# Optimization experiments

Measured on AMD Instinct MI355X. Metric: run time of the kernel, lower is better.

Reference implementation:

```python
import jax, jax.numpy as jnp
import numpy as np

B, C, H, W = 2, 256, 128, 128
G, S = 2, 4  # group_num, stride


def setup_inputs() -> dict:
    key = jax.random.key(0)
    ks = jax.random.split(key, 6)
    x = jax.random.normal(ks[0], (B, C, H, W), jnp.float32)
    qkv_w = jax.random.normal(ks[1], (C + C // 2, C), jnp.float32) * 0.02
    qkv_b = jax.random.normal(ks[2], (C + C // 2,), jnp.float32) * 0.02
    out_w = jax.random.normal(ks[3], (C, C), jnp.float32) * 0.02
    out_b = jax.random.normal(ks[4], (C,), jnp.float32) * 0.02
    gamma = jax.random.normal(ks[5], (1,), jnp.float32) * 0.1
    return {"x": x, "qkv_w": qkv_w, "qkv_b": qkv_b, "out_w": out_w,
            "out_b": out_b, "gamma": gamma, "mode": 0}


def reference(x, qkv_w, qkv_b, out_w, out_b, gamma, mode):
    b, c, h, w = x.shape
    g, s = G, S
    b1, c1, c2 = b * g, c // 4 // g, c // g
    h1, w1 = h // s, w // s
    n1, n = h1 * w1, h * w
    # 1x1 QKV conv
    qkv = jnp.einsum('oc,bchw->bohw', qkv_w, x) + qkv_b[None, :, None, None]
    Q = qkv[:, :c // 4]
    K = qkv[:, c // 4:c // 2]
    V = qkv[:, c // 2:]
    # avg_pool2d with kernel=stride=s (non-overlapping) via reshape-mean
    pool = lambda t: t.reshape(b, c // 4, h1, s, w1, s).mean(axis=(3, 5))
    q = pool(Q).reshape(b1, c1, n1)
    k = pool(K).reshape(b1, c1, n1)
    Qf = Q.reshape(b1, c1, n)
    Kf = K.reshape(b1, c1, n)
    Vf = V.reshape(b1, c2, n)
    # attention maps; softmax over dim=1 (the row / key index)
    A_c = jax.nn.softmax(jnp.einsum('bki,bkj->bij', k, Qf), axis=1)   # [b1,n1,n]
    A_m = jax.nn.softmax(jnp.einsum('bki,bkj->bij', k, q), axis=1)    # [b1,n1,n1]
    A_s = jax.nn.softmax(jnp.einsum('bki,bkj->bij', Kf, q), axis=1)   # [b1,n,n1]
    e = jnp.eye(n1, dtype=x.dtype)
    # E: each pooled-token identity row expanded over its s x s spatial block
    E = jnp.broadcast_to(e.reshape(n1, h1, 1, w1, 1),
                         (n1, h1, s, w1, s)).reshape(n1, n)
    A_c = jnp.linalg.inv(A_m + e) @ (A_c + E)                          # [b1,n1,n]
    O = (Vf @ A_s) @ A_c                                               # [b1,c2,n]
    out = O.reshape(b, c, h, w)
    out = jnp.einsum('oc,bchw->bohw', out_w, out) + out_b[None, :, None, None]
    if mode == 0:
        out = gamma[0] * out + x
    return out
```

## Files before the change

### kernel.cpp

```cpp
#include <hip/hip_runtime.h>
#include <cstdint>
#include <cstddef>

#define HWN 16384
#define NP1 1024
#define RL2E 1.44269504f

typedef __attribute__((ext_vector_type(8))) short bf16x8;
typedef __attribute__((ext_vector_type(8))) unsigned short ushort8v;
typedef __attribute__((ext_vector_type(4))) unsigned short ushort4v;
typedef __attribute__((ext_vector_type(2))) unsigned int uint2v;
typedef __attribute__((ext_vector_type(4))) unsigned int uint4v;
typedef __attribute__((ext_vector_type(4))) float f32x4;

__device__ __forceinline__ unsigned short f2bu(float f) {
  unsigned int u = __builtin_bit_cast(unsigned int, f);
  u = (u + 0x7FFFu + ((u >> 16) & 1u)) >> 16;
  return (unsigned short)u;
}
__device__ __forceinline__ float b2f(unsigned short s) {
  unsigned int u = ((unsigned int)s) << 16;
  return __builtin_bit_cast(float, u);
}
__device__ __forceinline__ unsigned cvtpk(float lo, float hi) {
  unsigned r;
  asm("v_cvt_pk_bf16_f32 %0, %1, %2" : "=v"(r) : "v"(lo), "v"(hi));
  return r;
}
__device__ __forceinline__ bf16x8 scale_l2e(ushort8v t) {
  ushort8v o;
#pragma unroll
  for (int q = 0; q < 8; ++q) o[q] = f2bu(RL2E * b2f(t[q]));
  return __builtin_bit_cast(bf16x8, o);
}
#define MFMA16(A,B,C) __builtin_amdgcn_mfma_f32_16x16x32_bf16((A),(B),(C),0,0,0)
#define PIDX(r,c) ((((r) << 6) + (c)) ^ (((r) & 7) << 3))

__global__ __launch_bounds__(256) void k_cast(
    const float* __restrict__ x, const float* __restrict__ qkv_w,
    const float* __restrict__ out_w, unsigned short* __restrict__ xbT,
    unsigned short* __restrict__ wqb, unsigned short* __restrict__ wob) {
  int bid = blockIdx.x, t = threadIdx.x;
  if (bid < 2048) {
    __shared__ float Lt[64][65];
    int b = bid >> 10, rest = bid & 1023, ct = rest >> 8, pt = rest & 255;
    const float* xp = x + ((size_t)b * 256 + ct * 64) * HWN + pt * 64;
    for (int it = 0; it < 16; ++it) {
      int idx = it * 256 + t; int cc = idx >> 6, pp = idx & 63;
      Lt[cc][pp] = xp[(size_t)cc * HWN + pp];
    }
    __syncthreads();
    int prow = t >> 2, c0 = (t & 3) * 16;
    unsigned short* dst = xbT + ((size_t)b * HWN + pt * 64 + prow) * 256 + ct * 64 + c0;
    uint4v o1, o2;
#pragma unroll
    for (int q = 0; q < 4; ++q) o1[q] = cvtpk(Lt[c0 + 2*q][prow], Lt[c0 + 2*q + 1][prow]);
#pragma unroll
    for (int q = 0; q < 4; ++q) o2[q] = cvtpk(Lt[c0 + 8 + 2*q][prow], Lt[c0 + 9 + 2*q][prow]);
    *(uint4v*)dst = o1;
    *(uint4v*)(dst + 8) = o2;
  } else {
    int base = (bid - 2048) * 1024 + t * 4;
    if (base < 98304) {
      float4 v = *(const float4*)(qkv_w + base);
      uint2v o; o[0] = cvtpk(v.x, v.y); o[1] = cvtpk(v.z, v.w);
      *(uint2v*)(wqb + base) = o;
    } else {
      int b2 = base - 98304;
      float4 v = *(const float4*)(out_w + b2);
      uint2v o; o[0] = cvtpk(v.x, v.y); o[1] = cvtpk(v.z, v.w);
      *(uint2v*)(wob + b2) = o;
    }
  }
}

__global__ __launch_bounds__(256) void k_qkv(
    const unsigned short* __restrict__ wqb, const unsigned short* __restrict__ xbT,
    const float* __restrict__ qkv_b, unsigned short* __restrict__ qkvb,
    unsigned short* __restrict__ kT) {
  int pt = blockIdx.x, b = blockIdx.y;
  int tid = threadIdx.x, w = tid >> 6, lane = tid & 63;
  int lg = lane >> 4, ln = lane & 15;
  f32x4 acc[6][4] = {};
#pragma unroll
  for (int ks = 0; ks < 8; ++ks) {
    int c0 = ks * 32;
    bf16x8 bx[4];
#pragma unroll
    for (int nt = 0; nt < 4; ++nt)
      bx[nt] = *(const bf16x8*)(xbT + ((size_t)b * HWN + pt * 64 + nt * 16 + ln) * 256 + c0 + lg * 8);
#pragma unroll
    for (int ot = 0; ot < 6; ++ot) {
      bf16x8 aw = *(const bf16x8*)(wqb + (size_t)(ot * 64 + w * 16 + ln) * 256 + c0 + lg * 8);
#pragma unroll
      for (int nt = 0; nt < 4; ++nt)
        acc[ot][nt] = MFMA16(aw, bx[nt], acc[ot][nt]);
    }
  }
#pragma unroll
  for (int ot = 0; ot < 6; ++ot) {
    int ob = ot * 64 + w * 16 + lg * 4;
    float b0 = qkv_b[ob], b1 = qkv_b[ob + 1], b2 = qkv_b[ob + 2], b3 = qkv_b[ob + 3];
#pragma unroll
    for (int nt = 0; nt < 4; ++nt) {
      int p = pt * 64 + nt * 16 + ln;
      unsigned u01 = cvtpk(acc[ot][nt][0] + b0, acc[ot][nt][1] + b1);
      unsigned u23 = cvtpk(acc[ot][nt][2] + b2, acc[ot][nt][3] + b3);
      size_t qb = ((size_t)b * 384 + ob) * HWN + p;
      qkvb[qb]           = (unsigned short)u01;
      qkvb[qb + HWN]     = (unsigned short)(u01 >> 16);
      qkvb[qb + 2 * HWN] = (unsigned short)u23;
      qkvb[qb + 3 * HWN] = (unsigned short)(u23 >> 16);
      if (ot == 1) {
        int bgi = b * 2 + (w >> 1);
        int d0 = (w & 1) * 16 + lg * 4;
        uint2v kv; kv[0] = u01; kv[1] = u23;
        *(uint2v*)(kT + ((size_t)bgi * HWN + p) * 32 + d0) = kv;
      }
    }
  }
}

__global__ __launch_bounds__(256) void k_pool(
    const unsigned short* __restrict__ qkvb, unsigned short* __restrict__ qpb,
    unsigned short* __restrict__ kpt) {
  int idx = blockIdx.x * 256 + threadIdx.x;
  int i1 = idx & 1023, cc = (idx >> 10) & 31, bg = idx >> 15;
  int b = bg >> 1, g = bg & 1;
  int h1 = i1 >> 5, w1 = i1 & 31;
  const unsigned short* bq = qkvb + (size_t)(b * 384 + g * 32 + cc) * HWN;
  const unsigned short* bk = qkvb + (size_t)(b * 384 + 64 + g * 32 + cc) * HWN;
  float sq = 0.f, sk = 0.f;
#pragma unroll
  for (int sh = 0; sh < 4; ++sh) {
    int off = (h1 * 4 + sh) * 128 + w1 * 4;
    ushort4v vq = *(const ushort4v*)(bq + off);
    ushort4v vk = *(const ushort4v*)(bk + off);
#pragma unroll
    for (int e = 0; e < 4; ++e) { sq += b2f(vq[e]); sk += b2f(vk[e]); }
  }
  qpb[((size_t)bg * 32 + cc) * NP1 + i1] = f2bu(sq * 0.0625f);
  kpt[((size_t)bg * NP1 + i1) * 32 + cc] = f2bu(sk * 0.0625f);
}

__global__ __launch_bounds__(256) void k_fw1s(
    const unsigned short* __restrict__ qkvb, const unsigned short* __restrict__ kT,
    const unsigned short* __restrict__ qpb, const unsigned short* __restrict__ kpt,
    float* __restrict__ pacc, float* __restrict__ pl,
    unsigned short* __restrict__ Eut, float* __restrict__ lpart) {
  __shared__ unsigned short PtS[2][64 * 64];
  __shared__ float redL[4][64];
  int n = blockIdx.x;
  int tid = threadIdx.x, w = tid >> 6, lane = tid & 63;
  int lg = lane >> 4, ln = lane & 15;

  if (n < 512) {
    int wid = ((n & 7) << 6) + (n >> 3);
    int jt = wid & 15, kc = (wid >> 4) & 7, bg = wid >> 7;
    int b = bg >> 1, g = bg & 1;
    const int Vch = b * 384 + 128 + g * 128;
    bf16x8 bq[4];
#pragma unroll
    for (int nt = 0; nt < 4; ++nt) {
      ushort8v t8;
#pragma unroll
      for (int jr = 0; jr < 8; ++jr)
        t8[jr] = qpb[((size_t)bg * 32 + lg * 8 + jr) * NP1 + jt * 64 + nt * 16 + ln];
      bq[nt] = scale_l2e(t8);
    }
    f32x4 acc[2][4] = {};
    float lsum[4] = {0.f, 0.f, 0.f, 0.f};
    const int i0base = kc * 2048;
    const unsigned short* kTbase = kT + ((size_t)bg * HWN + i0base + w * 16 + ln) * 32 + lg * 8;
    const unsigned short* Vrow0 = qkvb + (size_t)(Vch + w * 32 + ln) * HWN + i0base + lg * 8;
    const unsigned short* Vrow1 = qkvb + (size_t)(Vch + w * 32 + 16 + ln) * HWN + i0base + lg * 8;

    bf16x8 akA, akB;
    bf16x8 avA[4], avB[4];
    akA = *(const bf16x8*)(kTbase);
    {
      f32x4 sn[4];
#pragma unroll
      for (int nt = 0; nt < 4; ++nt) { f32x4 z = {0.f,0.f,0.f,0.f}; sn[nt] = MFMA16(akA, bq[nt], z); }
      akB = *(const bf16x8*)(kTbase + 2048);
      avA[0] = *(const bf16x8*)(Vrow0);
      avA[1] = *(const bf16x8*)(Vrow1);
      avA[2] = *(const bf16x8*)(Vrow0 + 32);
      avA[3] = *(const bf16x8*)(Vrow1 + 32);
#pragma unroll
      for (int nt = 0; nt < 4; ++nt) {
        float e0 = exp2f(sn[nt][0]), e1 = exp2f(sn[nt][1]), e2 = exp2f(sn[nt][2]), e3 = exp2f(sn[nt][3]);
        lsum[nt] += (e0 + e1) + (e2 + e3);
        uint2v pk; pk[0] = cvtpk(e0, e1); pk[1] = cvtpk(e2, e3);
        *(uint2v*)&PtS[0][PIDX(nt * 16 + ln, w * 16 + lg * 4)] = pk;
      }
    }
    for (int pr = 0; pr < 16; ++pr) {
      int c = pr * 2;
      __syncthreads();
      f32x4 sn[4];
#pragma unroll
      for (int nt = 0; nt < 4; ++nt) { f32x4 z = {0.f,0.f,0.f,0.f}; sn[nt] = MFMA16(akB, bq[nt], z); }
      {
        int c2 = (c + 2) & 31, c1 = c + 1;
        akA = *(const bf16x8*)(kTbase + (size_t)c2 * 2048);
        avB[0] = *(const bf16x8*)(Vrow0 + c1 * 64);
        avB[1] = *(const bf16x8*)(Vrow1 + c1 * 64);
        avB[2] = *(const bf16x8*)(Vrow0 + c1 * 64 + 32);
        avB[3] = *(const bf16x8*)(Vrow1 + c1 * 64 + 32);
      }
      __builtin_amdgcn_s_setprio(1);
#pragma unroll
      for (int ist = 0; ist < 2; ++ist) {
        bf16x8 bp[4];
#pragma unroll
        for (int nt = 0; nt < 4; ++nt)
          bp[nt] = *(const bf16x8*)&PtS[0][PIDX(nt * 16 + ln, ist * 32 + lg * 8)];
#pragma unroll
        for (int nt = 0; nt < 4; ++nt) {
          acc[0][nt] = MFMA16(avA[ist * 2 + 0], bp[nt], acc[0][nt]);
          acc[1][nt] = MFMA16(avA[ist * 2 + 1], bp[nt], acc[1][nt]);
        }
      }
      __builtin_amdgcn_s_setprio(0);
#pragma unroll
      for (int nt = 0; nt < 4; ++nt) {
        float e0 = exp2f(sn[nt][0]), e1 = exp2f(sn[nt][1]), e2 = exp2f(sn[nt][2]), e3 = exp2f(sn[nt][3]);
        lsum[nt] += (e0 + e1) + (e2 + e3);
        uint2v pk; pk[0] = cvtpk(e0, e1); pk[1] = cvtpk(e2, e3);
        *(uint2v*)&PtS[1][PIDX(nt * 16 + ln, w * 16 + lg * 4)] = pk;
      }
      __syncthreads();
      if (pr < 15) {
#pragma unroll
        for (int nt = 0; nt < 4; ++nt) { f32x4 z = {0.f,0.f,0.f,0.f}; sn[nt] = MFMA16(akA, bq[nt], z); }
        int c3 = c + 3, c2 = c + 2;
        akB = *(const bf16x8*)(kTbase + (size_t)c3 * 2048);
        avA[0] = *(const bf16x8*)(Vrow0 + c2 * 64);
        avA[1] = *(const bf16x8*)(Vrow1 + c2 * 64);
        avA[2] = *(const bf16x8*)(Vrow0 + c2 * 64 + 32);
        avA[3] = *(const bf16x8*)(Vrow1 + c2 * 64 + 32);
      }
      __builtin_amdgcn_s_setprio(1);
#pragma unroll
      for (int ist = 0; ist < 2; ++ist) {
        bf16x8 bp[4];
#pragma unroll
        for (int nt = 0; nt < 4; ++nt)
          bp[nt] = *(const bf16x8*)&PtS[1][PIDX(nt * 16 + ln, ist * 32 + lg * 8)];
#pragma unroll
        for (int nt = 0; nt < 4; ++nt) {
          acc[0][nt] = MFMA16(avB[ist * 2 + 0], bp[nt], acc[0][nt]);
          acc[1][nt] = MFMA16(avB[ist * 2 + 1], bp[nt], acc[1][nt]);
        }
      }
      __builtin_amdgcn_s_setprio(0);
      if (pr < 15) {
#pragma unroll
        for (int nt = 0; nt < 4; ++nt) {
          float e0 = exp2f(sn[nt][0]), e1 = exp2f(sn[nt][1]), e2 = exp2f(sn[nt][2]), e3 = exp2f(sn[nt][3]);
          lsum[nt] += (e0 + e1) + (e2 + e3);
          uint2v pk; pk[0] = cvtpk(e0, e1); pk[1] = cvtpk(e2, e3);
          *(uint2v*)&PtS[0][PIDX(nt * 16 + ln, w * 16 + lg * 4)] = pk;
        }
      }
    }
    size_t pb = (((size_t)bg * 16 + jt) * 8 + kc) * 8192;
#pragma unroll
    for (int ct = 0; ct < 2; ++ct)
#pragma unroll
      for (int nt = 0; nt < 4; ++nt)
#pragma unroll
        for (int r = 0; r < 4; ++r)
          pacc[pb + (size_t)(w * 32 + ct * 16 + lg * 4 + r) * 64 + nt * 16 + ln] = acc[ct][nt][r];
#pragma unroll
    for (int nt = 0; nt < 4; ++nt) {
      float v = lsum[nt];
      v += __shfl_xor(v, 16); v += __shfl_xor(v, 32);
      if (lane < 16) redL[w][nt * 16 + lane] = v;
    }
    __syncthreads();
    if (tid < 64)
      pl[(((size_t)bg * 16 + jt) * 8 + kc) * 64 + tid] =
          redL[0][tid] + redL[1][tid] + redL[2][tid] + redL[3][tid];
  } else {
    int n2 = n - 512;
    int jt = n2 & 15, ic = (n2 >> 4) & 3, bg = n2 >> 6;
    bf16x8 bq[4];
#pragma unroll
    for (int nt = 0; nt < 4; ++nt) {
      ushort8v t8;
#pragma unroll
      for (int jr = 0; jr < 8; ++jr)
        t8[jr] = qpb[((size_t)bg * 32 + lg * 8 + jr) * NP1 + jt * 64 + nt * 16 + ln];
      bq[nt] = scale_l2e(t8);
    }
    float lsum[4] = {0.f, 0.f, 0.f, 0.f};
    for (int chk = 0; chk < 4; ++chk) {
      int i0 = ic * 256 + chk * 64;
      bf16x8 ak = *(const bf16x8*)(kpt + ((size_t)bg * NP1 + i0 + w * 16 + ln) * 32 + lg * 8);
#pragma unroll
      for (int nt = 0; nt < 4; ++nt) {
        f32x4 z = {0.f, 0.f, 0.f, 0.f};
        f32x4 s = MFMA16(ak, bq[nt], z);
        float e0 = exp2f(s[0]), e1 = exp2f(s[1]), e2 = exp2f(s[2]), e3 = exp2f(s[3]);
        lsum[nt] += (e0 + e1) + (e2 + e3);
        int j = jt * 64 + nt * 16 + ln;
        int ib = i0 + w * 16 + lg * 4;
        uint2v pk;
        pk[0] = cvtpk(e0, e1);
        pk[1] = cvtpk(e2, e3);
        *(uint2v*)(Eut + ((size_t)bg * NP1 + j) * NP1 + ib) = pk;
      }
    }
#pragma unroll
    for (int nt = 0; nt < 4; ++nt) {
      float v = lsum[nt];
      v += __shfl_xor(v, 16); v += __shfl_xor(v, 32);
      if (lane < 16) redL[w][nt * 16 + lane] = v;
    }
    __syncthreads();
    if (tid < 64)
      lpart[((size_t)(bg * 4 + ic)) * NP1 + jt * 64 + tid] =
          redL[0][tid] + redL[1][tid] + redL[2][tid] + redL[3][tid];
  }
}

__global__ __launch_bounds__(256) void k_comb2(
    const float* __restrict__ pacc, const float* __restrict__ pl,
    float* __restrict__ Yf, const unsigned short* __restrict__ Eut,
    const float* __restrict__ lpart, float* __restrict__ linv,
    float* __restrict__ rvecp) {
  int n = blockIdx.x, t = threadIdx.x;
  if (n < 2048) {
    int gid = n * 256 + t;
    int bg = gid >> 17, rem = gid & 131071;
    int c = rem >> 10, j = rem & 1023;
    int jt = j >> 6, jj = j & 63;
    float s = 0.f, l = 0.f;
#pragma unroll
    for (int kc = 0; kc < 8; ++kc) {
      size_t pb = ((size_t)bg * 16 + jt) * 8 + kc;
      s += pacc[pb * 8192 + c * 64 + jj];
      l += pl[pb * 64 + jj];
    }
    Yf[gid] = s / l;
  } else {
    __shared__ float linv_s[32];
    int n2 = n - 2048;
    int jc = n2 & 31, bg = n2 >> 5;
    if (t < 32) {
      int j = jc * 32 + t;
      float l = lpart[((size_t)(bg * 4 + 0)) * NP1 + j] + lpart[((size_t)(bg * 4 + 1)) * NP1 + j] +
                lpart[((size_t)(bg * 4 + 2)) * NP1 + j] + lpart[((size_t)(bg * 4 + 3)) * NP1 + j];
      float inv = 1.f / l;
      linv_s[t] = inv;
      linv[(size_t)bg * NP1 + j] = inv;
    }
    __syncthreads();
    int i0 = t * 4;
    float a0 = 0.f, a1 = 0.f, a2 = 0.f, a3 = 0.f;
#pragma unroll 8
    for (int jj = 0; jj < 32; ++jj) {
      float li = linv_s[jj];
      ushort4v e4 = *(const ushort4v*)(Eut + ((size_t)bg * NP1 + jc * 32 + jj) * NP1 + i0);
      a0 += b2f(e4[0]) * li; a1 += b2f(e4[1]) * li;
      a2 += b2f(e4[2]) * li; a3 += b2f(e4[3]) * li;
    }
    float4 o = {a0, a1, a2, a3};
    *(float4*)(rvecp + ((size_t)(jc * 4 + bg)) * NP1 + i0) = o;
  }
}

__global__ __launch_bounds__(256) void k_proj(
    const float* __restrict__ rvecp, float* __restrict__ Yf,
    unsigned short* __restrict__ U0b) {
  int ct = blockIdx.x, bg = blockIdx.y, t = threadIdx.x;
  __shared__ float rs[1024];
  __shared__ float red[256];
  __shared__ float crow[8];
  __shared__ float sSs;
  for (int j = t; j < 1024; j += 256) {
    float s = 0.f;
#pragma unroll
    for (int p = 0; p < 32; ++p) s += rvecp[((size_t)(p * 4 + bg)) * NP1 + j];
    rs[j] = s;
  }
  __syncthreads();
  float p = rs[t] + rs[t + 256] + rs[t + 512] + rs[t + 768];
  red[t] = p; __syncthreads();
  for (int s = 128; s > 0; s >>= 1) {
    if (t < s) red[t] += red[t + s];
    __syncthreads();
  }
  if (t == 0) sSs = red[0];
  __syncthreads();
  int row = t >> 5, ln32 = t & 31;
  const float* yrow = Yf + ((size_t)(bg * 128 + ct * 8 + row)) * NP1;
  float a = 0.f;
  for (int j = ln32; j < 1024; j += 32) a += yrow[j] * rs[j];
#pragma unroll
  for (int m = 1; m <= 16; m <<= 1) a += __shfl_xor(a, m, 32);
  if (ln32 == 0) crow[row] = a / sSs;
  __syncthreads();
  for (int e = t; e < 8 * 1024; e += 256) {
    int rr = e >> 10, j = e & 1023;
    size_t o = ((size_t)(bg * 128 + ct * 8 + rr)) * NP1 + j;
    float y = Yf[o], cv = crow[rr];
    Yf[o] = y - 0.5f * cv;
    U0b[o] = f2bu(y - cv);
  }
}

__global__ __launch_bounds__(256) void k_neu(
    const unsigned short* __restrict__ Vin, const unsigned short* __restrict__ Eut,
    const float* __restrict__ linv, const float* __restrict__ W2f,
    unsigned short* __restrict__ W2b) {
  int jt = blockIdx.x, ct = blockIdx.y, bg = blockIdx.z;
  int tid = threadIdx.x, w = tid >> 6, lane = tid & 63;
  int lg = lane >> 4, ln = lane & 15;
  int j0 = jt * 32, c0 = ct * 64 + w * 16;
  f32x4 acc[2] = {};
  for (int ks = 0; ks < 32; ++ks) {
    int i0 = ks * 32;
    bf16x8 a = *(const bf16x8*)(Vin + ((size_t)(bg * 128) + c0 + ln) * NP1 + i0 + lg * 8);
#pragma unroll
    for (int nt = 0; nt < 2; ++nt) {
      bf16x8 bt = *(const bf16x8*)(Eut + ((size_t)bg * NP1 + j0 + nt * 16 + ln) * NP1 + i0 + lg * 8);
      acc[nt] = MFMA16(a, bt, acc[nt]);
    }
  }
#pragma unroll
  for (int nt = 0; nt < 2; ++nt) {
    int j = j0 + nt * 16 + ln;
    float li = linv[(size_t)bg * NP1 + j];
#pragma unroll
    for (int r = 0; r < 4; ++r) {
      size_t o = ((size_t)(bg * 128) + c0 + lg * 4 + r) * NP1 + j;
      W2b[o] = f2bu(W2f[o] - acc[nt][r] * li);
    }
  }
}

__global__ __launch_bounds__(256) void k_flashO(
    const unsigned short* __restrict__ qkvb, const unsigned short* __restrict__ kpt,
    const unsigned short* __restrict__ W2b, unsigned short* __restrict__ Ot) {
  int jt = blockIdx.x, bg = blockIdx.y;
  int b = bg >> 1, g = bg & 1;
  int tid = threadIdx.x, w = tid >> 6, lane = tid & 63;
  int lg = lane >> 4, ln = lane & 15;
  __shared__ unsigned short PtS[2][64 * 64];
  __shared__ float redL[4][64];
  __shared__ float smL[64];
  const int Qch = b * 384 + g * 32;
  bf16x8 bq[4];
#pragma unroll
  for (int nt = 0; nt < 4; ++nt) {
    ushort8v t8;
#pragma unroll
    for (int jr = 0; jr < 8; ++jr)
      t8[jr] = qkvb[(size_t)(Qch + lg * 8 + jr) * HWN + jt * 64 + nt * 16 + ln];
    bq[nt] = scale_l2e(t8);
  }
  f32x4 acc[2][4] = {};
  float lsum[4] = {0.f, 0.f, 0.f, 0.f};
  const unsigned short* kbase = kpt + ((size_t)bg * NP1 + w * 16 + ln) * 32 + lg * 8;
  const unsigned short* Wrow0 = W2b + ((size_t)bg * 128 + w * 32 + ln) * NP1 + lg * 8;
  const unsigned short* Wrow1 = W2b + ((size_t)bg * 128 + w * 32 + 16 + ln) * NP1 + lg * 8;

  bf16x8 akA, akB;
  bf16x8 avA[4], avB[4];
  akA = *(const bf16x8*)(kbase);
  {
    f32x4 sn[4];
#pragma unroll
    for (int nt = 0; nt < 4; ++nt) { f32x4 z = {0.f,0.f,0.f,0.f}; sn[nt] = MFMA16(akA, bq[nt], z); }
    akB = *(const bf16x8*)(kbase + 2048);
    avA[0] = *(const bf16x8*)(Wrow0);
    avA[1] = *(const bf16x8*)(Wrow1);
    avA[2] = *(const bf16x8*)(Wrow0 + 32);
    avA[3] = *(const bf16x8*)(Wrow1 + 32);
#pragma unroll
    for (int nt = 0; nt < 4; ++nt) {
      float e0 = exp2f(sn[nt][0]), e1 = exp2f(sn[nt][1]), e2 = exp2f(sn[nt][2]), e3 = exp2f(sn[nt][3]);
      lsum[nt] += (e0 + e1) + (e2 + e3);
      uint2v pk; pk[0] = cvtpk(e0, e1); pk[1] = cvtpk(e2, e3);
      *(uint2v*)&PtS[0][PIDX(nt * 16 + ln, w * 16 + lg * 4)] = pk;
    }
  }
  for (int pr = 0; pr < 8; ++pr) {
    int c = pr * 2;
    __syncthreads();
    f32x4 sn[4];
#pragma unroll
    for (int nt = 0; nt < 4; ++nt) { f32x4 z = {0.f,0.f,0.f,0.f}; sn[nt] = MFMA16(akB, bq[nt], z); }
    {
      int c2 = (c + 2) & 15, c1 = c + 1;
      akA = *(const bf16x8*)(kbase + (size_t)c2 * 2048);
      avB[0] = *(const bf16x8*)(Wrow0 + c1 * 64);
      avB[1] = *(const bf16x8*)(Wrow1 + c1 * 64);
      avB[2] = *(const bf16x8*)(Wrow0 + c1 * 64 + 32);
      avB[3] = *(const bf16x8*)(Wrow1 + c1 * 64 + 32);
    }
    __builtin_amdgcn_s_setprio(1);
#pragma unroll
    for (int ist = 0; ist < 2; ++ist) {
      bf16x8 bp[4];
#pragma unroll
      for (int nt = 0; nt < 4; ++nt)
        bp[nt] = *(const bf16x8*)&PtS[0][PIDX(nt * 16 + ln, ist * 32 + lg * 8)];
#pragma unroll
      for (int nt = 0; nt < 4; ++nt) {
        acc[0][nt] = MFMA16(avA[ist * 2 + 0], bp[nt], acc[0][nt]);
        acc[1][nt] = MFMA16(avA[ist * 2 + 1], bp[nt], acc[1][nt]);
      }
    }
    __builtin_amdgcn_s_setprio(0);
#pragma unroll
    for (int nt = 0; nt < 4; ++nt) {
      float e0 = exp2f(sn[nt][0]), e1 = exp2f(sn[nt][1]), e2 = exp2f(sn[nt][2]), e3 = exp2f(sn[nt][3]);
      lsum[nt] += (e0 + e1) + (e2 + e3);
      uint2v pk; pk[0] = cvtpk(e0, e1); pk[1] = cvtpk(e2, e3);
      *(uint2v*)&PtS[1][PIDX(nt * 16 + ln, w * 16 + lg * 4)] = pk;
    }
    __syncthreads();
    if (pr < 7) {
#pragma unroll
      for (int nt = 0; nt < 4; ++nt) { f32x4 z = {0.f,0.f,0.f,0.f}; sn[nt] = MFMA16(akA, bq[nt], z); }
      int c3 = c + 3, c2 = c + 2;
      akB = *(const bf16x8*)(kbase + (size_t)c3 * 2048);
      avA[0] = *(const bf16x8*)(Wrow0 + c2 * 64);
      avA[1] = *(const bf16x8*)(Wrow1 + c2 * 64);
      avA[2] = *(const bf16x8*)(Wrow0 + c2 * 64 + 32);
      avA[3] = *(const bf16x8*)(Wrow1 + c2 * 64 + 32);
    }
    __builtin_amdgcn_s_setprio(1);
#pragma unroll
    for (int ist = 0; ist < 2; ++ist) {
      bf16x8 bp[4];
#pragma unroll
      for (int nt = 0; nt < 4; ++nt)
        bp[nt] = *(const bf16x8*)&PtS[1][PIDX(nt * 16 + ln, ist * 32 + lg * 8)];
#pragma unroll
      for (int nt = 0; nt < 4; ++nt) {
        acc[0][nt] = MFMA16(avB[ist * 2 + 0], bp[nt], acc[0][nt]);
        acc[1][nt] = MFMA16(avB[ist * 2 + 1], bp[nt], acc[1][nt]);
      }
    }
    __builtin_amdgcn_s_setprio(0);
    if (pr < 7) {
#pragma unroll
      for (int nt = 0; nt < 4; ++nt) {
        float e0 = exp2f(sn[nt][0]), e1 = exp2f(sn[nt][1]), e2 = exp2f(sn[nt][2]), e3 = exp2f(sn[nt][3]);
        lsum[nt] += (e0 + e1) + (e2 + e3);
        uint2v pk; pk[0] = cvtpk(e0, e1); pk[1] = cvtpk(e2, e3);
        *(uint2v*)&PtS[0][PIDX(nt * 16 + ln, w * 16 + lg * 4)] = pk;
      }
    }
  }
#pragma unroll
  for (int nt = 0; nt < 4; ++nt) {
    float v = lsum[nt];
    v += __shfl_xor(v, 16); v += __shfl_xor(v, 32);
    if (lane < 16) redL[w][nt * 16 + lane] = v;
  }
  __syncthreads();
  if (tid < 64) smL[tid] = redL[0][tid] + redL[1][tid] + redL[2][tid] + redL[3][tid];
  __syncthreads();
#pragma unroll
  for (int nt = 0; nt < 4; ++nt) {
    int jj = nt * 16 + ln;
    int jg = jt * 64 + jj;
    float li = 1.f / smL[jj];
    int i1 = (jg >> 9) * 32 + ((jg & 127) >> 2);
#pragma unroll
    for (int ct = 0; ct < 2; ++ct) {
      int c = w * 32 + ct * 16 + lg * 4;
      float v0 = acc[ct][nt][0] * li + b2f(W2b[((size_t)bg * 128 + c + 0) * NP1 + i1]);
      float v1 = acc[ct][nt][1] * li + b2f(W2b[((size_t)bg * 128 + c + 1) * NP1 + i1]);
      float v2 = acc[ct][nt][2] * li + b2f(W2b[((size_t)bg * 128 + c + 2) * NP1 + i1]);
      float v3 = acc[ct][nt][3] * li + b2f(W2b[((size_t)bg * 128 + c + 3) * NP1 + i1]);
      uint2v o2; o2[0] = cvtpk(v0, v1); o2[1] = cvtpk(v2, v3);
      *(uint2v*)(Ot + ((size_t)b * HWN + jg) * 256 + g * 128 + c) = o2;
    }
  }
}

__global__ __launch_bounds__(256) void k_out(
    const unsigned short* __restrict__ wob, const unsigned short* __restrict__ Ot,
    const float* __restrict__ out_b, const unsigned short* __restrict__ xbT,
    const float* __restrict__ gamma, const int* __restrict__ mode,
    float* __restrict__ out) {
  int pt = blockIdx.x, b = blockIdx.y;
  int tid = threadIdx.x, w = tid >> 6, lane = tid & 63;
  int lg = lane >> 4, ln = lane & 15;
  f32x4 acc[4][4] = {};
#pragma unroll
  for (int ks = 0; ks < 8; ++ks) {
    int c0 = ks * 32;
    bf16x8 bx[4];
#pragma unroll
    for (int nt = 0; nt < 4; ++nt)
      bx[nt] = *(const bf16x8*)(Ot + ((size_t)b * HWN + pt * 64 + nt * 16 + ln) * 256 + c0 + lg * 8);
#pragma unroll
    for (int h = 0; h < 4; ++h) {
      bf16x8 aw = *(const bf16x8*)(wob + (size_t)(h * 64 + w * 16 + ln) * 256 + c0 + lg * 8);
#pragma unroll
      for (int nt = 0; nt < 4; ++nt)
        acc[h][nt] = MFMA16(aw, bx[nt], acc[h][nt]);
    }
  }
  float gm = gamma[0];
  int md = mode[0];
#pragma unroll
  for (int h = 0; h < 4; ++h) {
    int o0 = h * 64 + w * 16 + lg * 4;
    float b0 = out_b[o0], b1 = out_b[o0 + 1], b2 = out_b[o0 + 2], b3 = out_b[o0 + 3];
#pragma unroll
    for (int nt = 0; nt < 4; ++nt) {
      int p = pt * 64 + nt * 16 + ln;
      ushort4v xr = *(const ushort4v*)(xbT + ((size_t)b * HWN + p) * 256 + o0);
      float v0 = acc[h][nt][0] + b0, v1 = acc[h][nt][1] + b1;
      float v2 = acc[h][nt][2] + b2, v3 = acc[h][nt][3] + b3;
      size_t off = ((size_t)b * 256 + o0) * HWN + p;
      if (md == 0) {
        out[off]           = gm * v0 + b2f(xr[0]);
        out[off + HWN]     = gm * v1 + b2f(xr[1]);
        out[off + 2 * HWN] = gm * v2 + b2f(xr[2]);
        out[off + 3 * HWN] = gm * v3 + b2f(xr[3]);
      } else {
        out[off]           = v0;
        out[off + HWN]     = v1;
        out[off + 2 * HWN] = v2;
        out[off + 3 * HWN] = v3;
      }
    }
  }
}

extern "C" void kernel_launch(void* const* d_in, const int* in_sizes, int n_in,
                              void* d_out, int out_size, void* d_ws, size_t ws_size,
                              hipStream_t stream) {
  (void)in_sizes; (void)n_in; (void)out_size;
  const float* x     = (const float*)d_in[0];
  const float* qkv_w = (const float*)d_in[1];
  const float* qkv_b = (const float*)d_in[2];
  const float* out_w = (const float*)d_in[3];
  const float* out_b = (const float*)d_in[4];
  const float* gamma = (const float*)d_in[5];
  const int*   mode  = (const int*)d_in[6];
  float* out = (float*)d_out;

  char* wsb = (char*)d_ws;
  size_t off = 0;
  auto alloc = [&](size_t bytes) { char* p = wsb + off; off += bytes; return p; };
  unsigned short* xbT  = (unsigned short*)alloc(16777216);
  unsigned short* wqb  = (unsigned short*)alloc(196608);
  unsigned short* wob  = (unsigned short*)alloc(131072);
  unsigned short* qkvb = (unsigned short*)alloc(25165824);
  unsigned short* kT   = (unsigned short*)alloc(4194304);
  unsigned short* qpb  = (unsigned short*)alloc(262144);
  unsigned short* kpt  = (unsigned short*)alloc(262144);
  unsigned short* Eut  = (unsigned short*)alloc(8388608);
  float*          lpart= (float*)alloc(65536);
  float*          linv = (float*)alloc(16384);
  float*          rvecp= (float*)alloc(524288);
  float*          pacc = (float*)alloc(16777216);
  float*          pl   = (float*)alloc(131072);
  float*          Yf   = (float*)alloc(2097152);
  unsigned short* U0b  = (unsigned short*)alloc(1048576);
  unsigned short* W2b  = (unsigned short*)alloc(1048576);
  unsigned short* Ot   = (unsigned short*)pacc;
  if (ws_size < off) return;

  k_cast<<<2208, 256, 0, stream>>>(x, qkv_w, out_w, xbT, wqb, wob);
  k_qkv<<<dim3(256, 2), 256, 0, stream>>>(wqb, xbT, qkv_b, qkvb, kT);
  k_pool<<<512, 256, 0, stream>>>(qkvb, qpb, kpt);
  k_fw1s<<<768, 256, 0, stream>>>(qkvb, kT, qpb, kpt, pacc, pl, Eut, lpart);
  k_comb2<<<2176, 256, 0, stream>>>(pacc, pl, Yf, Eut, lpart, linv, rvecp);
  k_proj<<<dim3(16, 4), 256, 0, stream>>>(rvecp, Yf, U0b);
  k_neu<<<dim3(32, 2, 4), 256, 0, stream>>>(U0b, Eut, linv, Yf, W2b);
  k_flashO<<<dim3(256, 4), 256, 0, stream>>>(qkvb, kpt, W2b, Ot);
  k_out<<<dim3(256, 2), 256, 0, stream>>>(wob, Ot, out_b, xbT, gamma, mode, out);
}
```

Baseline: 187.8 us.

## Rewrite flashO as single-wave 32x32 MFMA kernel with register-resident P

Replaces the 4-wave, 64-query flash kernel that staged softmax probabilities through double-buffered LDS with a single-wave, 32-query kernel using 32x32x16 bf16 MFMAs. Probabilities are repacked into MFMA operand layout with cross-half lane shuffles instead of LDS writes and reads, which removes most barriers. The cost is no software prefetch of K/W tiles, four times more W2 reads per query across more blocks, and scalar 2-byte output stores.

```diff
diff --git a/kernel.cpp b/kernel.cpp
--- a/kernel.cpp
+++ b/kernel.cpp
@@ -12,6 +12,7 @@
 typedef __attribute__((ext_vector_type(2))) unsigned int uint2v;
 typedef __attribute__((ext_vector_type(4))) unsigned int uint4v;
 typedef __attribute__((ext_vector_type(4))) float f32x4;
+typedef __attribute__((ext_vector_type(16))) float f32x16;
 
 __device__ __forceinline__ unsigned short f2bu(float f) {
   unsigned int u = __builtin_bit_cast(unsigned int, f);
@@ -34,6 +35,7 @@
   return __builtin_bit_cast(bf16x8, o);
 }
 #define MFMA16(A,B,C) __builtin_amdgcn_mfma_f32_16x16x32_bf16((A),(B),(C),0,0,0)
+#define MFMA32(A,B,C) __builtin_amdgcn_mfma_f32_32x32x16_bf16((A),(B),(C),0,0,0)
 #define PIDX(r,c) ((((r) << 6) + (c)) ^ (((r) & 7) << 3))
 
 __global__ __launch_bounds__(256) void k_cast(
@@ -442,146 +444,80 @@
   }
 }
 
-__global__ __launch_bounds__(256) void k_flashO(
+__global__ __launch_bounds__(64) void k_flashO(
     const unsigned short* __restrict__ qkvb, const unsigned short* __restrict__ kpt,
     const unsigned short* __restrict__ W2b, unsigned short* __restrict__ Ot) {
   int jt = blockIdx.x, bg = blockIdx.y;
   int b = bg >> 1, g = bg & 1;
-  int tid = threadIdx.x, w = tid >> 6, lane = tid & 63;
-  int lg = lane >> 4, ln = lane & 15;
-  __shared__ unsigned short PtS[2][64 * 64];
-  __shared__ float redL[4][64];
-  __shared__ float smL[64];
+  int lane = threadIdx.x;
+  int q32 = lane & 31, hi = lane >> 5;
+  __shared__ float sL[32];
   const int Qch = b * 384 + g * 32;
-  bf16x8 bq[4];
-#pragma unroll
-  for (int nt = 0; nt < 4; ++nt) {
+  const int qglob = jt * 32 + q32;
+  bf16x8 bq[2];
+#pragma unroll
+  for (int win = 0; win < 2; ++win) {
     ushort8v t8;
 #pragma unroll
-    for (int jr = 0; jr < 8; ++jr)
-      t8[jr] = qkvb[(size_t)(Qch + lg * 8 + jr) * HWN + jt * 64 + nt * 16 + ln];
-    bq[nt] = scale_l2e(t8);
-  }
-  f32x4 acc[2][4] = {};
-  float lsum[4] = {0.f, 0.f, 0.f, 0.f};
-  const unsigned short* kbase = kpt + ((size_t)bg * NP1 + w * 16 + ln) * 32 + lg * 8;
-  const unsigned short* Wrow0 = W2b + ((size_t)bg * 128 + w * 32 + ln) * NP1 + lg * 8;
-  const unsigned short* Wrow1 = W2b + ((size_t)bg * 128 + w * 32 + 16 + ln) * NP1 + lg * 8;
-
-  bf16x8 akA, akB;
-  bf16x8 avA[4], avB[4];
-  akA = *(const bf16x8*)(kbase);
-  {
-    f32x4 sn[4];
-#pragma unroll
-    for (int nt = 0; nt < 4; ++nt) { f32x4 z = {0.f,0.f,0.f,0.f}; sn[nt] = MFMA16(akA, bq[nt], z); }
-    akB = *(const bf16x8*)(kbase + 2048);
-    avA[0] = *(const bf16x8*)(Wrow0);
-    avA[1] = *(const bf16x8*)(Wrow1);
-    avA[2] = *(const bf16x8*)(Wrow0 + 32);
-    avA[3] = *(const bf16x8*)(Wrow1 + 32);
-#pragma unroll
-    for (int nt = 0; nt < 4; ++nt) {
-      float e0 = exp2f(sn[nt][0]), e1 = exp2f(sn[nt][1]), e2 = exp2f(sn[nt][2]), e3 = exp2f(sn[nt][3]);
-      lsum[nt] += (e0 + e1) + (e2 + e3);
-      uint2v pk; pk[0] = cvtpk(e0, e1); pk[1] = cvtpk(e2, e3);
-      *(uint2v*)&PtS[0][PIDX(nt * 16 + ln, w * 16 + lg * 4)] = pk;
-    }
-  }
-  for (int pr = 0; pr < 8; ++pr) {
-    int c = pr * 2;
-    __syncthreads();
-    f32x4 sn[4];
-#pragma unroll
-    for (int nt = 0; nt < 4; ++nt) { f32x4 z = {0.f,0.f,0.f,0.f}; sn[nt] = MFMA16(akB, bq[nt], z); }
-    {
-      int c2 = (c + 2) & 15, c1 = c + 1;
-      akA = *(const bf16x8*)(kbase + (size_t)c2 * 2048);
-      avB[0] = *(const bf16x8*)(Wrow0 + c1 * 64);
-      avB[1] = *(const bf16x8*)(Wrow1 + c1 * 64);
-      avB[2] = *(const bf16x8*)(Wrow0 + c1 * 64 + 32);
-      avB[3] = *(const bf16x8*)(Wrow1 + c1 * 64 + 32);
-    }
-    __builtin_amdgcn_s_setprio(1);
-#pragma unroll
-    for (int ist = 0; ist < 2; ++ist) {
-      bf16x8 bp[4];
-#pragma unroll
-      for (int nt = 0; nt < 4; ++nt)
-        bp[nt] = *(const bf16x8*)&PtS[0][PIDX(nt * 16 + ln, ist * 32 + lg * 8)];
-#pragma unroll
-      for (int nt = 0; nt < 4; ++nt) {
-        acc[0][nt] = MFMA16(avA[ist * 2 + 0], bp[nt], acc[0][nt]);
-        acc[1][nt] = MFMA16(avA[ist * 2 + 1], bp[nt], acc[1][nt]);
-      }
-    }
-    __builtin_amdgcn_s_setprio(0);
-#pragma unroll
-    for (int nt = 0; nt < 4; ++nt) {
-      float e0 = exp2f(sn[nt][0]), e1 = exp2f(sn[nt][1]), e2 = exp2f(sn[nt][2]), e3 = exp2f(sn[nt][3]);
-      lsum[nt] += (e0 + e1) + (e2 + e3);
-      uint2v pk; pk[0] = cvtpk(e0, e1); pk[1] = cvtpk(e2, e3);
-      *(uint2v*)&PtS[1][PIDX(nt * 16 + ln, w * 16 + lg * 4)] = pk;
-    }
-    __syncthreads();
-    if (pr < 7) {
-#pragma unroll
-      for (int nt = 0; nt < 4; ++nt) { f32x4 z = {0.f,0.f,0.f,0.f}; sn[nt] = MFMA16(akA, bq[nt], z); }
-      int c3 = c + 3, c2 = c + 2;
-      akB = *(const bf16x8*)(kbase + (size_t)c3 * 2048);
-      avA[0] = *(const bf16x8*)(Wrow0 + c2 * 64);
-      avA[1] = *(const bf16x8*)(Wrow1 + c2 * 64);
-      avA[2] = *(const bf16x8*)(Wrow0 + c2 * 64 + 32);
-      avA[3] = *(const bf16x8*)(Wrow1 + c2 * 64 + 32);
-    }
-    __builtin_amdgcn_s_setprio(1);
-#pragma unroll
-    for (int ist = 0; ist < 2; ++ist) {
-      bf16x8 bp[4];
-#pragma unroll
-      for (int nt = 0; nt < 4; ++nt)
-        bp[nt] = *(const bf16x8*)&PtS[1][PIDX(nt * 16 + ln, ist * 32 + lg * 8)];
-#pragma unroll
-      for (int nt = 0; nt < 4; ++nt) {
-        acc[0][nt] = MFMA16(avB[ist * 2 + 0], bp[nt], acc[0][nt]);
-        acc[1][nt] = MFMA16(avB[ist * 2 + 1], bp[nt], acc[1][nt]);
-      }
-    }
-    __builtin_amdgcn_s_setprio(0);
-    if (pr < 7) {
-#pragma unroll
-      for (int nt = 0; nt < 4; ++nt) {
-        float e0 = exp2f(sn[nt][0]), e1 = exp2f(sn[nt][1]), e2 = exp2f(sn[nt][2]), e3 = exp2f(sn[nt][3]);
-        lsum[nt] += (e0 + e1) + (e2 + e3);
-        uint2v pk; pk[0] = cvtpk(e0, e1); pk[1] = cvtpk(e2, e3);
-        *(uint2v*)&PtS[0][PIDX(nt * 16 + ln, w * 16 + lg * 4)] = pk;
-      }
-    }
-  }
-#pragma unroll
-  for (int nt = 0; nt < 4; ++nt) {
-    float v = lsum[nt];
-    v += __shfl_xor(v, 16); v += __shfl_xor(v, 32);
-    if (lane < 16) redL[w][nt * 16 + lane] = v;
-  }
+    for (int j = 0; j < 8; ++j)
+      t8[j] = qkvb[(size_t)(Qch + win * 16 + hi * 8 + j) * HWN + qglob];
+    bq[win] = scale_l2e(t8);
+  }
+  f32x16 acc[4] = {};
+  float lsum = 0.f;
+  const unsigned short* kb = kpt + (size_t)bg * NP1 * 32;
+  const unsigned short* Wb = W2b + (size_t)bg * 128 * NP1;
+  const f32x16 zz = {};
+  for (int i0 = 0; i0 < 1024; i0 += 32) {
+    bf16x8 ak0 = *(const bf16x8*)(kb + (size_t)(i0 + q32) * 32 + hi * 8);
+    bf16x8 ak1 = *(const bf16x8*)(kb + (size_t)(i0 + q32) * 32 + 16 + hi * 8);
+    f32x16 s = MFMA32(ak0, bq[0], zz);
+    s = MFMA32(ak1, bq[1], s);
+    float p[16];
+#pragma unroll
+    for (int r = 0; r < 16; ++r) p[r] = exp2f(s[r]);
+#pragma unroll
+    for (int r = 0; r < 16; ++r) lsum += p[r];
+    unsigned d[8], sw[8];
+#pragma unroll
+    for (int m = 0; m < 8; ++m) d[m] = cvtpk(p[2 * m], p[2 * m + 1]);
+#pragma unroll
+    for (int m = 0; m < 8; ++m) sw[m] = (unsigned)__shfl_xor((int)d[m], 32);
+    uint4v w0, w1;
+    w0[0] = hi ? sw[2] : d[0];
+    w0[1] = hi ? sw[3] : d[1];
+    w0[2] = hi ? d[2] : sw[0];
+    w0[3] = hi ? d[3] : sw[1];
+    w1[0] = hi ? sw[6] : d[4];
+    w1[1] = hi ? sw[7] : d[5];
+    w1[2] = hi ? d[6] : sw[4];
+    w1[3] = hi ? d[7] : sw[5];
+    bf16x8 pa0 = __builtin_bit_cast(bf16x8, w0);
+    bf16x8 pa1 = __builtin_bit_cast(bf16x8, w1);
+#pragma unroll
+    for (int ct = 0; ct < 4; ++ct) {
+      const unsigned short* wr = Wb + (size_t)(ct * 32 + q32) * NP1 + i0;
+      bf16x8 bv0 = *(const bf16x8*)(wr + hi * 8);
+      bf16x8 bv1 = *(const bf16x8*)(wr + 16 + hi * 8);
+      acc[ct] = MFMA32(pa0, bv0, acc[ct]);
+      acc[ct] = MFMA32(pa1, bv1, acc[ct]);
+    }
+  }
+  lsum += __shfl_xor(lsum, 32);
+  sL[q32] = lsum;
   __syncthreads();
-  if (tid < 64) smL[tid] = redL[0][tid] + redL[1][tid] + redL[2][tid] + redL[3][tid];
-  __syncthreads();
-#pragma unroll
-  for (int nt = 0; nt < 4; ++nt) {
-    int jj = nt * 16 + ln;
-    int jg = jt * 64 + jj;
-    float li = 1.f / smL[jj];
-    int i1 = (jg >> 9) * 32 + ((jg & 127) >> 2);
-#pragma unroll
-    for (int ct = 0; ct < 2; ++ct) {
-      int c = w * 32 + ct * 16 + lg * 4;
-      float v0 = acc[ct][nt][0] * li + b2f(W2b[((size_t)bg * 128 + c + 0) * NP1 + i1]);
-      float v1 = acc[ct][nt][1] * li + b2f(W2b[((size_t)bg * 128 + c + 1) * NP1 + i1]);
-      float v2 = acc[ct][nt][2] * li + b2f(W2b[((size_t)bg * 128 + c + 2) * NP1 + i1]);
-      float v3 = acc[ct][nt][3] * li + b2f(W2b[((size_t)bg * 128 + c + 3) * NP1 + i1]);
-      uint2v o2; o2[0] = cvtpk(v0, v1); o2[1] = cvtpk(v2, v3);
-      *(uint2v*)(Ot + ((size_t)b * HWN + jg) * 256 + g * 128 + c) = o2;
+#pragma unroll
+  for (int ct = 0; ct < 4; ++ct) {
+    int chl = ct * 32 + q32;
+    int chg = g * 128 + chl;
+#pragma unroll
+    for (int r = 0; r < 16; ++r) {
+      int qrow = (r & 3) + 8 * (r >> 2) + 4 * hi;
+      int qg = jt * 32 + qrow;
+      float li = 1.f / sL[qrow];
+      int i1 = (qg >> 9) * 32 + ((qg & 127) >> 2);
+      float v = acc[ct][r] * li + b2f(W2b[((size_t)bg * 128 + chl) * NP1 + i1]);
+      Ot[((size_t)b * HWN + qg) * 256 + chg] = f2bu(v);
     }
   }
 }
@@ -680,6 +616,6 @@
   k_comb2<<<2176, 256, 0, stream>>>(pacc, pl, Yf, Eut, lpart, linv, rvecp);
   k_proj<<<dim3(16, 4), 256, 0, stream>>>(rvecp, Yf, U0b);
   k_neu<<<dim3(32, 2, 4), 256, 0, stream>>>(U0b, Eut, linv, Yf, W2b);
-  k_flashO<<<dim3(256, 4), 256, 0, stream>>>(qkvb, kpt, W2b, Ot);
+  k_flashO<<<dim3(512, 4), 64, 0, stream>>>(qkvb, kpt, W2b, Ot);
   k_out<<<dim3(256, 2), 256, 0, stream>>>(wob, Ot, out_b, xbT, gamma, mode, out);
 }
```

Result: slower. 228.1 us (+21.5%).
